# Kernel optimization log

Hardware: AMD Instinct MI355X
Metric: run time of the kernel (lower is better)

Reference implementation:

```python
import jax, jax.numpy as jnp
import numpy as np

B, S, D, H, FD = 2, 2048, 1024, 16, 64
DK = D // H
ALPHA = 1.0


def _l2norm(t):
    # matches F.normalize(p=2, dim=-1): divide by max(norm, eps)
    n = jnp.linalg.norm(t, axis=-1, keepdims=True)
    return t / jnp.maximum(n, 1e-12)


def setup_inputs() -> dict:
    key = jax.random.key(0)
    ks = jax.random.split(key, 12)
    sc = 0.02
    return {
        "x": jax.random.normal(ks[0], (B, S, D), jnp.float32),
        "features": jax.random.normal(ks[1], (B, S, FD), jnp.float32),
        "requirements": jax.random.normal(ks[2], (B, S, FD), jnp.float32),
        "Wq": jax.random.normal(ks[3], (D, D), jnp.float32) * sc,
        "bq": jnp.zeros((D,), jnp.float32),
        "Wk": jax.random.normal(ks[4], (D, D), jnp.float32) * sc,
        "bk": jnp.zeros((D,), jnp.float32),
        "Wv": jax.random.normal(ks[5], (D, D), jnp.float32) * sc,
        "bv": jnp.zeros((D,), jnp.float32),
        "Wo": jax.random.normal(ks[6], (D, D), jnp.float32) * sc,
        "bo": jnp.zeros((D,), jnp.float32),
        "pos_ids": jax.random.randint(ks[7], (B, S), 0, 8),
        "causal_mask": jnp.tril(jnp.ones((S, S), bool)),
    }


def reference(x, features, requirements, Wq, bq, Wk, bk, Wv, bv, Wo, bo,
              pos_ids, causal_mask):
    # q/k/v projections -> [B, S, H, DK]
    Q = (x @ Wq + bq).reshape(B, S, H, DK)
    K = (x @ Wk + bk).reshape(B, S, H, DK)
    V = (x @ Wv + bv).reshape(B, S, H, DK)

    # scaled QK^T: [B, H, S, S]
    scores = jnp.einsum('bshd,bthd->bhst', Q, K) / np.sqrt(DK).astype(np.float32)

    # ASA bias (features_only mode): cosine compat req_i . feat_j -> [B, S, S]
    bias = jnp.einsum('bsf,btf->bst', _l2norm(requirements), _l2norm(features))
    scores = scores + ALPHA * bias[:, None, :, :]

    # causal mask (True = allowed)
    scores = jnp.where(causal_mask[None, None, :, :], scores, -jnp.inf)

    weights = jax.nn.softmax(scores, axis=-1)
    weights = jnp.nan_to_num(weights, nan=0.0)

    out = jnp.einsum('bhst,bthd->bshd', weights, V).reshape(B, S, D)
    return out @ Wo + bo
```

## Files before the change

kernel.cpp:

```cpp
#include <hip/hip_runtime.h>
#include <hip/hip_bf16.h>
#include <math.h>

#define Bb 2
#define Ss 2048
#define Dd 1024
#define Hh 16
#define DK 64
#define FD 64

#define LOG2E 1.4426950408889634f

typedef short short8 __attribute__((ext_vector_type(8)));
typedef float f32x4 __attribute__((ext_vector_type(4)));

static __device__ inline ushort f2bf(float f) {
    union { float f; unsigned u; } v; v.f = f;
    unsigned r = v.u + 0x7FFF + ((v.u >> 16) & 1);
    return (ushort)(r >> 16);
}

static __device__ inline uint cvt_pk_bf16(float lo, float hi) {
    uint r;
    asm("v_cvt_pk_bf16_f32 %0, %1, %2" : "=v"(r) : "v"(lo), "v"(hi));
    return r;
}
static __device__ inline float fexp2(float x) {
    return __builtin_amdgcn_exp2f(x);
}

__global__ __launch_bounds__(256) void cast_bf16(const float* __restrict__ in,
                                                 ushort* __restrict__ out) {
    size_t p = (size_t)blockIdx.x * 256 + threadIdx.x;
    float2 v = *(const float2*)(in + 2 * p);
    ((uint*)out)[p] = (uint)f2bf(v.x) | ((uint)f2bf(v.y) << 16);
}

__global__ __launch_bounds__(256) void transpose_cast4(const float* __restrict__ W0,
                                                       const float* __restrict__ W1,
                                                       const float* __restrict__ W2,
                                                       const float* __restrict__ W3,
                                                       ushort* __restrict__ WT) {
    __shared__ float T[64][65];
    const float* W = blockIdx.z == 0 ? W0 : blockIdx.z == 1 ? W1 : blockIdx.z == 2 ? W2 : W3;
    ushort* dst = WT + (size_t)blockIdx.z * Dd * Dd;
    const int k0 = blockIdx.x * 64, n0 = blockIdx.y * 64;
    const int tid = threadIdx.x;
#pragma unroll
    for (int i = 0; i < 4; ++i) {
        int kr = i * 16 + (tid >> 4);
        int nc = (tid & 15) * 4;
        float4 v = *(const float4*)(W + (size_t)(k0 + kr) * Dd + n0 + nc);
        T[kr][nc] = v.x; T[kr][nc + 1] = v.y; T[kr][nc + 2] = v.z; T[kr][nc + 3] = v.w;
    }
    __syncthreads();
    int nr = tid >> 2;
    int kc = (tid & 3) * 16;
    uint pk[8];
#pragma unroll
    for (int j = 0; j < 8; ++j)
        pk[j] = (uint)f2bf(T[kc + 2 * j][nr]) | ((uint)f2bf(T[kc + 2 * j + 1][nr]) << 16);
    uint* o = (uint*)(dst + (size_t)(n0 + nr) * Dd + k0 + kc);
    *(int4*)o = *(int4*)&pk[0];
    *(int4*)(o + 4) = *(int4*)&pk[4];
}

__global__ __launch_bounds__(256) void l2norm2(const float* __restrict__ fsrc,
                                               const float* __restrict__ rsrc,
                                               float* __restrict__ fn,
                                               float* __restrict__ rn) {
    int row = blockIdx.x * 4 + (threadIdx.x >> 6);
    int lane = threadIdx.x & 63;
    const float* in = fsrc; float* out = fn; int r = row;
    if (row >= Bb * Ss) { in = rsrc; out = rn; r = row - Bb * Ss; }
    float v = in[(size_t)r * FD + lane];
    float s = v * v;
#pragma unroll
    for (int off = 32; off; off >>= 1) s += __shfl_xor(s, off, 64);
    out[(size_t)r * FD + lane] = v / fmaxf(sqrtf(s), 1e-12f);
}

__global__ __launch_bounds__(256) void pack_aux(const float* __restrict__ rn,
                                                const float* __restrict__ fn,
                                                ushort* __restrict__ Qext,
                                                ushort* __restrict__ Kext) {
    size_t p = (size_t)blockIdx.x * 256 + threadIdx.x;
    int j = (int)(p & 31);
    size_t row = p >> 5;
    int s = (int)(row & (Ss - 1));
    int bh = (int)(row >> 11);
    int b = bh >> 4;
    size_t src = ((size_t)(b * Ss + s)) * FD + j * 2;
    float2 r2 = *(const float2*)(rn + src);
    float2 f2 = *(const float2*)(fn + src);
    ((uint*)Qext)[row * 64 + 32 + j] =
        (uint)f2bf(r2.x * LOG2E) | ((uint)f2bf(r2.y * LOG2E) << 16);
    ((uint*)Kext)[row * 64 + 32 + j] = (uint)f2bf(f2.x) | ((uint)f2bf(f2.y) << 16);
}

__global__ __launch_bounds__(256) void pack_vt(const ushort* __restrict__ Vrow,
                                               ushort* __restrict__ Vt) {
    __shared__ ushort T[64][72];
    const int tid = threadIdx.x;
    const int s0 = blockIdx.x * 64;
    const int h = blockIdx.y, b = blockIdx.z;
#pragma unroll
    for (int i = 0; i < 2; ++i) {
        int f = tid + i * 256;
        int sr = f >> 3, dc = (f & 7) * 8;
        *(int4*)&T[sr][dc] =
            *(const int4*)(Vrow + ((size_t)((b * Hh + h) * Ss) + s0 + sr) * 64 + dc);
    }
    __syncthreads();
    int d = tid >> 2;
    int sg = (tid & 3) * 16;
    uint pk[8];
#pragma unroll
    for (int j = 0; j < 8; ++j)
        pk[j] = (uint)T[sg + 2 * j][d] | ((uint)T[sg + 2 * j + 1][d] << 16);
    uint* dst = (uint*)(Vt + ((size_t)((b * Hh + h) * DK + d)) * Ss + s0 + sg);
    *(int4*)dst = *(int4*)&pk[0];
    *(int4*)(dst + 4) = *(int4*)&pk[4];
}

__global__ __launch_bounds__(256) void gemm_qkv(const ushort* __restrict__ xb,
                                                const ushort* __restrict__ WT,
                                                const float* __restrict__ bq,
                                                const float* __restrict__ bk,
                                                const float* __restrict__ bv,
                                                ushort* __restrict__ Qext,
                                                ushort* __restrict__ Kext,
                                                ushort* __restrict__ Vrow) {
    __shared__ ushort smem[2][128][72];
    ushort (*As)[72] = smem[0];
    ushort (*Bs)[72] = smem[1];
    const int tid = threadIdx.x;
    const int lane = tid & 63, wave = tid >> 6;
    const int col = lane & 15, quad = lane >> 4;
    const int wm = wave >> 1, wn = wave & 1;
    const int id = blockIdx.x >> 3;
    const int n0 = (blockIdx.x & 7) * 128;
    const int m0 = blockIdx.y * 128;
    const ushort* BTw = WT + (size_t)id * Dd * Dd;
    const float* bias = id == 0 ? bq : id == 1 ? bk : bv;

    f32x4 acc[4][4] = {};

    for (int k0 = 0; k0 < Dd; k0 += 64) {
        __syncthreads();
#pragma unroll
        for (int i = 0; i < 4; ++i) {
            int f = tid + i * 256;
            int r = f >> 3, c = (f & 7) * 8;
            *(int4*)&As[r][c] = *(const int4*)(xb + (size_t)(m0 + r) * Dd + k0 + c);
            *(int4*)&Bs[r][c] = *(const int4*)(BTw + (size_t)(n0 + r) * Dd + k0 + c);
        }
        __syncthreads();
#pragma unroll
        for (int kk = 0; kk < 2; ++kk) {
            short8 af[4], bf[4];
#pragma unroll
            for (int i = 0; i < 4; ++i) {
                af[i] = *(const short8*)&As[wm * 64 + i * 16 + col][kk * 32 + quad * 8];
                bf[i] = *(const short8*)&Bs[wn * 64 + i * 16 + col][kk * 32 + quad * 8];
            }
#pragma unroll
            for (int i = 0; i < 4; ++i)
#pragma unroll
                for (int j = 0; j < 4; ++j)
                    acc[i][j] = __builtin_amdgcn_mfma_f32_16x16x32_bf16(af[i], bf[j], acc[i][j], 0, 0, 0);
        }
    }

    __syncthreads();
    ushort (*Ep)[136] = (ushort (*)[136])&smem[0][0][0];
    const float scl = (id == 0) ? 0.125f * LOG2E : 1.0f;
#pragma unroll
    for (int j = 0; j < 4; ++j) {
        int n_local = wn * 64 + j * 16 + col;
        float bvl = bias[n0 + n_local];
#pragma unroll
        for (int i = 0; i < 4; ++i) {
            int mb = wm * 64 + i * 16 + quad * 4;
#pragma unroll
            for (int reg = 0; reg < 4; ++reg)
                Ep[mb + reg][n_local] = f2bf((acc[i][j][reg] + bvl) * scl);
        }
    }
    __syncthreads();
    {
        const int mrow = tid >> 1;
        const int half = tid & 1;
        const int b = m0 >> 11, s = (m0 & (Ss - 1)) + mrow;
        const int hh = (n0 >> 6) + half;
        if (id == 2) {
            ushort* drow = Vrow + ((size_t)(b * Hh + hh) * Ss + s) * 64;
#pragma unroll
            for (int k = 0; k < 8; ++k)
                *(int4*)(drow + k * 8) = *(int4*)&Ep[mrow][half * 64 + k * 8];
        } else {
            ushort* drow = (id == 0 ? Qext : Kext) + ((size_t)(b * Hh + hh) * Ss + s) * 128;
#pragma unroll
            for (int k = 0; k < 8; ++k)
                *(int4*)(drow + k * 8) = *(int4*)&Ep[mrow][half * 64 + k * 8];
        }
    }
}

__global__ __launch_bounds__(256) void gemm_out(const ushort* __restrict__ Ab,
                                                const ushort* __restrict__ BT,
                                                const float* __restrict__ bias,
                                                float* __restrict__ C) {
    __shared__ ushort As[128][72];
    __shared__ ushort Bs[128][72];
    const int tid = threadIdx.x;
    const int lane = tid & 63, wave = tid >> 6;
    const int col = lane & 15, quad = lane >> 4;
    const int wm = wave >> 1, wn = wave & 1;
    const int n0 = blockIdx.x * 128;
    const int m0 = blockIdx.y * 128;

    f32x4 acc[4][4] = {};

    for (int k0 = 0; k0 < Dd; k0 += 64) {
        __syncthreads();
#pragma unroll
        for (int i = 0; i < 4; ++i) {
            int f = tid + i * 256;
            int r = f >> 3, c = (f & 7) * 8;
            *(int4*)&As[r][c] = *(const int4*)(Ab + (size_t)(m0 + r) * Dd + k0 + c);
            *(int4*)&Bs[r][c] = *(const int4*)(BT + (size_t)(n0 + r) * Dd + k0 + c);
        }
        __syncthreads();
#pragma unroll
        for (int kk = 0; kk < 2; ++kk) {
            short8 af[4], bf[4];
#pragma unroll
            for (int i = 0; i < 4; ++i) {
                af[i] = *(const short8*)&As[wm * 64 + i * 16 + col][kk * 32 + quad * 8];
                bf[i] = *(const short8*)&Bs[wn * 64 + i * 16 + col][kk * 32 + quad * 8];
            }
#pragma unroll
            for (int i = 0; i < 4; ++i)
#pragma unroll
                for (int j = 0; j < 4; ++j)
                    acc[i][j] = __builtin_amdgcn_mfma_f32_16x16x32_bf16(af[i], bf[j], acc[i][j], 0, 0, 0);
        }
    }

#pragma unroll
    for (int j = 0; j < 4; ++j) {
        int n = n0 + wn * 64 + j * 16 + col;
        float bvl = bias[n];
#pragma unroll
        for (int i = 0; i < 4; ++i) {
#pragma unroll
            for (int reg = 0; reg < 4; ++reg) {
                int m = m0 + wm * 64 + i * 16 + quad * 4 + reg;
                C[(size_t)m * Dd + n] = acc[i][j][reg] + bvl;
            }
        }
    }
}

#define ABQ 128

__global__ __launch_bounds__(512) void attn_mfma8(const ushort* __restrict__ Qe,
                                                  const ushort* __restrict__ Ke,
                                                  const ushort* __restrict__ Vt,
                                                  ushort* __restrict__ Ob) {
    __shared__ ushort Ks[64][128];
    __shared__ ushort Vts[64][64];
    __shared__ ushort PsT[8][16][64];

    const int tid = threadIdx.x;
    const int wave = tid >> 6, lane = tid & 63;
    const int col = lane & 15, quad = lane >> 4;

    const int id = blockIdx.x;
    const int rep = id >> 8;
    const int slot = id & 255;
    const int bh = slot >> 3;
    const int qh = slot & 7;
    const int qt = rep ? qh : (15 - qh);
    const int b = bh >> 4, h = bh & 15;
    const int q0 = qt * ABQ;
    const int rowb = q0 + wave * 16;

    short8 qf[4];
    {
        const ushort* qp = Qe + ((size_t)bh * Ss + rowb + col) * 128 + quad * 8;
#pragma unroll
        for (int k0 = 0; k0 < 4; ++k0) qf[k0] = *(const short8*)(qp + k0 * 32);
    }

    const f32x4 zero4 = {0.f, 0.f, 0.f, 0.f};
    f32x4 oaccT[4] = {zero4, zero4, zero4, zero4};
    float lsum = 0.f;

    const ushort* Kbase = Ke + (size_t)bh * Ss * 128;
    const ushort* Vbase = Vt + (size_t)bh * 64 * Ss;
    const int xsw = col & 7;

    const int kr0 = tid >> 4, kg0 = tid & 15;
    ushort* ksd0 = &Ks[kr0][(kg0 ^ (kr0 & 7)) * 8];
    ushort* ksd1 = &Ks[kr0 + 32][(kg0 ^ ((kr0 + 32) & 7)) * 8];
    const ushort* ksrc0 = Kbase + (size_t)kr0 * 128 + kg0 * 8;
    const ushort* ksrc1 = Kbase + (size_t)(kr0 + 32) * 128 + kg0 * 8;
    const int vd = tid >> 3, vg = tid & 7;
    ushort* vsd = &Vts[vd][(vg ^ (vd & 7)) * 8];
    const ushort* vsrc = Vbase + (size_t)vd * Ss + vg * 8;

    const int ntiles = 2 * qt + 2;
    for (int t = 0; t < ntiles; ++t) {
        const int j0 = t * 64;
        __syncthreads();
        *(int4*)ksd0 = *(const int4*)ksrc0;   ksrc0 += 64 * 128;
        *(int4*)ksd1 = *(const int4*)ksrc1;   ksrc1 += 64 * 128;
        *(int4*)vsd  = *(const int4*)vsrc;    vsrc  += 64;
        __syncthreads();

        if (j0 > rowb + 15) continue;

        f32x4 sacc[4] = {zero4, zero4, zero4, zero4};
#pragma unroll
        for (int c = 0; c < 4; ++c)
#pragma unroll
            for (int k0 = 0; k0 < 4; ++k0) {
                short8 kf = *(const short8*)&Ks[c * 16 + col][((k0 * 4 + quad) ^ xsw) * 8];
                sacc[c] = __builtin_amdgcn_mfma_f32_16x16x32_bf16(kf, qf[k0], sacc[c], 0, 0, 0);
            }

        const bool diag = (j0 + 63 >= rowb);
        if (diag) {
            const int qrow_rel = rowb + col - j0;
#pragma unroll
            for (int c = 0; c < 4; ++c)
#pragma unroll
                for (int reg = 0; reg < 4; ++reg) {
                    float s = sacc[c][reg];
                    if (c * 16 + quad * 4 + reg > qrow_rel) s = -1e9f;
                    float p = fexp2(fminf(s, 28.853901f));
                    lsum += p;
                    sacc[c][reg] = p;
                }
        } else {
#pragma unroll
            for (int c = 0; c < 4; ++c)
#pragma unroll
                for (int reg = 0; reg < 4; ++reg) {
                    float p = fexp2(fminf(sacc[c][reg], 28.853901f));
                    lsum += p;
                    sacc[c][reg] = p;
                }
        }
#pragma unroll
        for (int c = 0; c < 4; ++c) {
            uint2 pk;
            pk.x = cvt_pk_bf16(sacc[c][0], sacc[c][1]);
            pk.y = cvt_pk_bf16(sacc[c][2], sacc[c][3]);
            *(uint2*)&PsT[wave][col][((c * 2 + (quad >> 1)) ^ xsw) * 8 + (quad & 1) * 4] = pk;
        }

#pragma unroll
        for (int k0 = 0; k0 < 2; ++k0) {
            short8 ptf = *(const short8*)&PsT[wave][col][((k0 * 4 + quad) ^ xsw) * 8];
#pragma unroll
            for (int c2 = 0; c2 < 4; ++c2) {
                short8 vtf = *(const short8*)&Vts[c2 * 16 + col][((k0 * 4 + quad) ^ xsw) * 8];
                oaccT[c2] = __builtin_amdgcn_mfma_f32_16x16x32_bf16(vtf, ptf, oaccT[c2], 0, 0, 0);
            }
        }
    }

    {
        float l = lsum;
        l += __shfl_xor(l, 16, 64);
        l += __shfl_xor(l, 32, 64);
        const float inv = 1.f / l;
        ushort* dst = Ob + ((size_t)b * Ss + rowb + col) * Dd + h * DK + quad * 4;
#pragma unroll
        for (int c2 = 0; c2 < 4; ++c2) {
            uint2 pk;
            pk.x = cvt_pk_bf16(oaccT[c2][0] * inv, oaccT[c2][1] * inv);
            pk.y = cvt_pk_bf16(oaccT[c2][2] * inv, oaccT[c2][3] * inv);
            *(uint2*)(dst + c2 * 16) = pk;
        }
    }
}

extern "C" void kernel_launch(void* const* d_in, const int* in_sizes, int n_in,
                              void* d_out, int out_size, void* d_ws, size_t ws_size,
                              hipStream_t stream) {
    const float* x            = (const float*)d_in[0];
    const float* features     = (const float*)d_in[1];
    const float* requirements = (const float*)d_in[2];
    const float* Wq = (const float*)d_in[3];
    const float* bq = (const float*)d_in[4];
    const float* Wk = (const float*)d_in[5];
    const float* bk = (const float*)d_in[6];
    const float* Wv = (const float*)d_in[7];
    const float* bv = (const float*)d_in[8];
    const float* Wo = (const float*)d_in[9];
    const float* bo = (const float*)d_in[10];

    float* out = (float*)d_out;
    float* ws = (float*)d_ws;

    ushort* xb   = (ushort*)(ws);
    ushort* WT   = (ushort*)(ws + 2097152);
    ushort* Qext = (ushort*)(ws + 4194304);
    ushort* Kext = (ushort*)(ws + 8388608);
    ushort* Vrow = (ushort*)(ws + 12582912);
    ushort* Vt   = (ushort*)(ws + 16777216);
    float*  fn   =           ws + 18874368;
    float*  rn   =           ws + 19136512;
    ushort* abb  = (ushort*)(ws + 12582912);

    cast_bf16<<<8192, 256, 0, stream>>>(x, xb);
    transpose_cast4<<<dim3(16, 16, 4), 256, 0, stream>>>(Wq, Wk, Wv, Wo, WT);
    l2norm2<<<2048, 256, 0, stream>>>(features, requirements, fn, rn);
    pack_aux<<<8192, 256, 0, stream>>>(rn, fn, Qext, Kext);

    gemm_qkv<<<dim3(24, 32), 256, 0, stream>>>(xb, WT, bq, bk, bv, Qext, Kext, Vrow);
    pack_vt<<<dim3(Ss / 64, Hh, Bb), 256, 0, stream>>>(Vrow, Vt);

    attn_mfma8<<<dim3(512), 512, 0, stream>>>(Qext, Kext, Vt, abb);

    gemm_out<<<dim3(8, 32), 256, 0, stream>>>(abb, WT + (size_t)3 * Dd * Dd, bo, out);
}
```

Measured before the change: 244.8 us.

## Give each attention wave two 16-row query tiles to reuse K/V fragments

The attention kernel now runs with 4 waves of 256 threads instead of 8 waves, and each wave handles 32 query rows as two 16-row sub-tiles. Each K and V fragment read from LDS feeds two MFMAs, which halves LDS fragment reads per unit of compute, and the cooperative K/V tile load is spread over fewer threads with more loads each. The cost is higher register pressure, fewer waves to hide latency, and coarser causal skipping, since a wave now skips a tile only when both sub-tiles are fully masked.

```diff
diff --git a/kernel.cpp b/kernel.cpp
--- a/kernel.cpp
+++ b/kernel.cpp
@@ -265,13 +265,13 @@
 
 #define ABQ 128
 
-__global__ __launch_bounds__(512) void attn_mfma8(const ushort* __restrict__ Qe,
-                                                  const ushort* __restrict__ Ke,
-                                                  const ushort* __restrict__ Vt,
-                                                  ushort* __restrict__ Ob) {
+__global__ __launch_bounds__(256) void attn_mfma11(const ushort* __restrict__ Qe,
+                                                   const ushort* __restrict__ Ke,
+                                                   const ushort* __restrict__ Vt,
+                                                   ushort* __restrict__ Ob) {
     __shared__ ushort Ks[64][128];
     __shared__ ushort Vts[64][64];
-    __shared__ ushort PsT[8][16][64];
+    __shared__ ushort PsT[4][2][16][64];
 
     const int tid = threadIdx.x;
     const int wave = tid >> 6, lane = tid & 63;
@@ -285,96 +285,144 @@
     const int qt = rep ? qh : (15 - qh);
     const int b = bh >> 4, h = bh & 15;
     const int q0 = qt * ABQ;
-    const int rowb = q0 + wave * 16;
-
-    short8 qf[4];
+    const int rowb = q0 + wave * 32;
+
+    short8 qf0[4], qf1[4];
     {
         const ushort* qp = Qe + ((size_t)bh * Ss + rowb + col) * 128 + quad * 8;
 #pragma unroll
-        for (int k0 = 0; k0 < 4; ++k0) qf[k0] = *(const short8*)(qp + k0 * 32);
+        for (int k0 = 0; k0 < 4; ++k0) {
+            qf0[k0] = *(const short8*)(qp + k0 * 32);
+            qf1[k0] = *(const short8*)(qp + 16 * 128 + k0 * 32);
+        }
     }
 
     const f32x4 zero4 = {0.f, 0.f, 0.f, 0.f};
-    f32x4 oaccT[4] = {zero4, zero4, zero4, zero4};
-    float lsum = 0.f;
+    f32x4 oacc0[4] = {zero4, zero4, zero4, zero4};
+    f32x4 oacc1[4] = {zero4, zero4, zero4, zero4};
+    float lsum0 = 0.f, lsum1 = 0.f;
 
     const ushort* Kbase = Ke + (size_t)bh * Ss * 128;
     const ushort* Vbase = Vt + (size_t)bh * 64 * Ss;
     const int xsw = col & 7;
 
-    const int kr0 = tid >> 4, kg0 = tid & 15;
-    ushort* ksd0 = &Ks[kr0][(kg0 ^ (kr0 & 7)) * 8];
-    ushort* ksd1 = &Ks[kr0 + 32][(kg0 ^ ((kr0 + 32) & 7)) * 8];
-    const ushort* ksrc0 = Kbase + (size_t)kr0 * 128 + kg0 * 8;
-    const ushort* ksrc1 = Kbase + (size_t)(kr0 + 32) * 128 + kg0 * 8;
-    const int vd = tid >> 3, vg = tid & 7;
-    ushort* vsd = &Vts[vd][(vg ^ (vd & 7)) * 8];
-    const ushort* vsrc = Vbase + (size_t)vd * Ss + vg * 8;
+    const int kr = tid >> 4, kg = tid & 15;
+    const int vr = tid >> 3, vg = tid & 7;
 
     const int ntiles = 2 * qt + 2;
     for (int t = 0; t < ntiles; ++t) {
         const int j0 = t * 64;
         __syncthreads();
-        *(int4*)ksd0 = *(const int4*)ksrc0;   ksrc0 += 64 * 128;
-        *(int4*)ksd1 = *(const int4*)ksrc1;   ksrc1 += 64 * 128;
-        *(int4*)vsd  = *(const int4*)vsrc;    vsrc  += 64;
-        __syncthreads();
-
-        if (j0 > rowb + 15) continue;
-
-        f32x4 sacc[4] = {zero4, zero4, zero4, zero4};
+        {
+            const ushort* kp = Kbase + (size_t)j0 * 128;
+            const ushort* vp = Vbase + j0;
+#pragma unroll
+            for (int i = 0; i < 4; ++i) {
+                int r = i * 16 + kr;
+                *(int4*)&Ks[r][(kg ^ (r & 7)) * 8] =
+                    *(const int4*)(kp + (size_t)r * 128 + kg * 8);
+            }
+#pragma unroll
+            for (int i = 0; i < 2; ++i) {
+                int r = i * 32 + vr;
+                *(int4*)&Vts[r][(vg ^ (r & 7)) * 8] =
+                    *(const int4*)(vp + (size_t)r * Ss + vg * 8);
+            }
+        }
+        __syncthreads();
+
+        if (j0 > rowb + 31) continue;
+
+        f32x4 s0[4] = {zero4, zero4, zero4, zero4};
+        f32x4 s1[4] = {zero4, zero4, zero4, zero4};
 #pragma unroll
         for (int c = 0; c < 4; ++c)
 #pragma unroll
             for (int k0 = 0; k0 < 4; ++k0) {
                 short8 kf = *(const short8*)&Ks[c * 16 + col][((k0 * 4 + quad) ^ xsw) * 8];
-                sacc[c] = __builtin_amdgcn_mfma_f32_16x16x32_bf16(kf, qf[k0], sacc[c], 0, 0, 0);
-            }
-
-        const bool diag = (j0 + 63 >= rowb);
-        if (diag) {
-            const int qrow_rel = rowb + col - j0;
-#pragma unroll
-            for (int c = 0; c < 4; ++c)
-#pragma unroll
-                for (int reg = 0; reg < 4; ++reg) {
-                    float s = sacc[c][reg];
-                    if (c * 16 + quad * 4 + reg > qrow_rel) s = -1e9f;
-                    float p = fexp2(fminf(s, 28.853901f));
-                    lsum += p;
-                    sacc[c][reg] = p;
-                }
-        } else {
-#pragma unroll
-            for (int c = 0; c < 4; ++c)
-#pragma unroll
-                for (int reg = 0; reg < 4; ++reg) {
-                    float p = fexp2(fminf(sacc[c][reg], 28.853901f));
-                    lsum += p;
-                    sacc[c][reg] = p;
-                }
-        }
-#pragma unroll
-        for (int c = 0; c < 4; ++c) {
-            uint2 pk;
-            pk.x = cvt_pk_bf16(sacc[c][0], sacc[c][1]);
-            pk.y = cvt_pk_bf16(sacc[c][2], sacc[c][3]);
-            *(uint2*)&PsT[wave][col][((c * 2 + (quad >> 1)) ^ xsw) * 8 + (quad & 1) * 4] = pk;
+                s0[c] = __builtin_amdgcn_mfma_f32_16x16x32_bf16(kf, qf0[k0], s0[c], 0, 0, 0);
+                s1[c] = __builtin_amdgcn_mfma_f32_16x16x32_bf16(kf, qf1[k0], s1[c], 0, 0, 0);
+            }
+
+        {
+            if (j0 + 63 >= rowb) {
+                const int qrr = rowb + col - j0;
+#pragma unroll
+                for (int c = 0; c < 4; ++c)
+#pragma unroll
+                    for (int reg = 0; reg < 4; ++reg) {
+                        float s = s0[c][reg];
+                        if (c * 16 + quad * 4 + reg > qrr) s = -1e9f;
+                        float p = fexp2(fminf(s, 28.853901f));
+                        lsum0 += p;
+                        s0[c][reg] = p;
+                    }
+            } else {
+#pragma unroll
+                for (int c = 0; c < 4; ++c)
+#pragma unroll
+                    for (int reg = 0; reg < 4; ++reg) {
+                        float p = fexp2(fminf(s0[c][reg], 28.853901f));
+                        lsum0 += p;
+                        s0[c][reg] = p;
+                    }
+            }
+#pragma unroll
+            for (int c = 0; c < 4; ++c) {
+                uint2 pk;
+                pk.x = cvt_pk_bf16(s0[c][0], s0[c][1]);
+                pk.y = cvt_pk_bf16(s0[c][2], s0[c][3]);
+                *(uint2*)&PsT[wave][0][col][((c * 2 + (quad >> 1)) ^ xsw) * 8 + (quad & 1) * 4] = pk;
+            }
+        }
+        {
+            const int rbs = rowb + 16;
+            if (j0 + 63 >= rbs) {
+                const int qrr = rbs + col - j0;
+#pragma unroll
+                for (int c = 0; c < 4; ++c)
+#pragma unroll
+                    for (int reg = 0; reg < 4; ++reg) {
+                        float s = s1[c][reg];
+                        if (c * 16 + quad * 4 + reg > qrr) s = -1e9f;
+                        float p = fexp2(fminf(s, 28.853901f));
+                        lsum1 += p;
+                        s1[c][reg] = p;
+                    }
+            } else {
+#pragma unroll
+                for (int c = 0; c < 4; ++c)
+#pragma unroll
+                    for (int reg = 0; reg < 4; ++reg) {
+                        float p = fexp2(fminf(s1[c][reg], 28.853901f));
+                        lsum1 += p;
+                        s1[c][reg] = p;
+                    }
+            }
+#pragma unroll
+            for (int c = 0; c < 4; ++c) {
+                uint2 pk;
+                pk.x = cvt_pk_bf16(s1[c][0], s1[c][1]);
+                pk.y = cvt_pk_bf16(s1[c][2], s1[c][3]);
+                *(uint2*)&PsT[wave][1][col][((c * 2 + (quad >> 1)) ^ xsw) * 8 + (quad & 1) * 4] = pk;
+            }
         }
 
 #pragma unroll
         for (int k0 = 0; k0 < 2; ++k0) {
-            short8 ptf = *(const short8*)&PsT[wave][col][((k0 * 4 + quad) ^ xsw) * 8];
+            short8 pt0 = *(const short8*)&PsT[wave][0][col][((k0 * 4 + quad) ^ xsw) * 8];
+            short8 pt1 = *(const short8*)&PsT[wave][1][col][((k0 * 4 + quad) ^ xsw) * 8];
 #pragma unroll
             for (int c2 = 0; c2 < 4; ++c2) {
                 short8 vtf = *(const short8*)&Vts[c2 * 16 + col][((k0 * 4 + quad) ^ xsw) * 8];
-                oaccT[c2] = __builtin_amdgcn_mfma_f32_16x16x32_bf16(vtf, ptf, oaccT[c2], 0, 0, 0);
+                oacc0[c2] = __builtin_amdgcn_mfma_f32_16x16x32_bf16(vtf, pt0, oacc0[c2], 0, 0, 0);
+                oacc1[c2] = __builtin_amdgcn_mfma_f32_16x16x32_bf16(vtf, pt1, oacc1[c2], 0, 0, 0);
             }
         }
     }
 
     {
-        float l = lsum;
+        float l = lsum0;
         l += __shfl_xor(l, 16, 64);
         l += __shfl_xor(l, 32, 64);
         const float inv = 1.f / l;
@@ -382,8 +430,22 @@
 #pragma unroll
         for (int c2 = 0; c2 < 4; ++c2) {
             uint2 pk;
-            pk.x = cvt_pk_bf16(oaccT[c2][0] * inv, oaccT[c2][1] * inv);
-            pk.y = cvt_pk_bf16(oaccT[c2][2] * inv, oaccT[c2][3] * inv);
+            pk.x = cvt_pk_bf16(oacc0[c2][0] * inv, oacc0[c2][1] * inv);
+            pk.y = cvt_pk_bf16(oacc0[c2][2] * inv, oacc0[c2][3] * inv);
+            *(uint2*)(dst + c2 * 16) = pk;
+        }
+    }
+    {
+        float l = lsum1;
+        l += __shfl_xor(l, 16, 64);
+        l += __shfl_xor(l, 32, 64);
+        const float inv = 1.f / l;
+        ushort* dst = Ob + ((size_t)b * Ss + rowb + 16 + col) * Dd + h * DK + quad * 4;
+#pragma unroll
+        for (int c2 = 0; c2 < 4; ++c2) {
+            uint2 pk;
+            pk.x = cvt_pk_bf16(oacc1[c2][0] * inv, oacc1[c2][1] * inv);
+            pk.y = cvt_pk_bf16(oacc1[c2][2] * inv, oacc1[c2][3] * inv);
             *(uint2*)(dst + c2 * 16) = pk;
         }
     }
@@ -425,7 +487,7 @@
     gemm_qkv<<<dim3(24, 32), 256, 0, stream>>>(xb, WT, bq, bk, bv, Qext, Kext, Vrow);
     pack_vt<<<dim3(Ss / 64, Hh, Bb), 256, 0, stream>>>(Vrow, Vt);
 
-    attn_mfma8<<<dim3(512), 512, 0, stream>>>(Qext, Kext, Vt, abb);
+    attn_mfma11<<<dim3(512), 256, 0, stream>>>(Qext, Kext, Vt, abb);
 
     gemm_out<<<dim3(8, 32), 256, 0, stream>>>(abb, WT + (size_t)3 * Dd * Dd, bo, out);
 }
```

Result: slower. 260.9 us (+6.6%).
